# Kernel tuning notes

Measured on AMD Instinct MI355X. Metric: run time of the kernel, lower is better.

## Reference

```python
import jax, jax.numpy as jnp
import numpy as np

B, M, K = 32, 64, 36
DS, DX, DQ, H = 512, 128, 512, 256


def setup_inputs() -> dict:
    key = jax.random.key(0)
    ks = jax.random.split(key, 11)
    sc = lambda fan_in: 1.0 / np.sqrt(fan_in)
    return {
        "s2": jax.random.normal(ks[0], (B, M, DS), jnp.float32),
        "x0": jax.random.normal(ks[1], (B, K, DX), jnp.float32),
        "q": jax.random.normal(ks[2], (B, DQ), jnp.float32),
        # score MLP: Linear(DS+DX+DQ -> H), ReLU, Linear(H -> 1)
        "score_w1": jax.random.normal(ks[3], (DS + DX + DQ, H), jnp.float32) * sc(DS + DX + DQ),
        "score_b1": jax.random.normal(ks[4], (H,), jnp.float32) * 0.01,
        "score_w2": jax.random.normal(ks[5], (H, 1), jnp.float32) * sc(H),
        "score_b2": jax.random.normal(ks[6], (1,), jnp.float32) * 0.01,
        # h MLP: Linear(DS -> H), ReLU, Linear(H -> DX)
        "h_w1": jax.random.normal(ks[7], (DS, H), jnp.float32) * sc(DS),
        "h_b1": jax.random.normal(ks[8], (H,), jnp.float32) * 0.01,
        "h_w2": jax.random.normal(ks[9], (H, DX), jnp.float32) * sc(H),
        "h_b2": jax.random.normal(ks[10], (DX,), jnp.float32) * 0.01,
    }


def reference(s2, x0, q, score_w1, score_b1, score_w2, score_b2, h_w1, h_b1, h_w2, h_b2):
    ds = s2.shape[-1]
    dx = x0.shape[-1]
    # First score Linear over concat [s_exp, x_exp, q_exp] decomposes into
    # block matmuls (same math as Linear on the concat, no 4D concat tensor).
    w_s = score_w1[:ds]            # (DS, H)
    w_x = score_w1[ds:ds + dx]     # (DX, H)
    w_q = score_w1[ds + dx:]       # (DQ, H)
    pre_s = jnp.einsum('bmd,dh->bmh', s2, w_s)   # (b, m, H)
    pre_x = jnp.einsum('bkd,dh->bkh', x0, w_x)   # (b, k, H)
    pre_q = q @ w_q                              # (b, H)
    hidden = jax.nn.relu(pre_s[:, :, None, :] + pre_x[:, None, :, :]
                         + pre_q[:, None, None, :] + score_b1)  # (b, m, k, H)
    logits = jnp.einsum('bmkh,h->bmk', hidden, score_w2[:, 0]) + score_b2[0]
    att = jax.nn.softmax(logits, axis=1)         # softmax over m
    h_s = jax.nn.relu(s2 @ h_w1 + h_b1) @ h_w2 + h_b2  # (b, m, DX)
    agg = jnp.einsum('bmk,bmf->bkf', att, h_s)   # (b, k, DX)
    return jnp.concatenate([x0, agg], axis=-1)   # (b, k, 2*DX)
```

## Files before the change

### kernel.cpp

```cpp
#include <hip/hip_runtime.h>

#define B_  32
#define M_  64
#define K_  36
#define DS_ 512
#define DX_ 128
#define DQ_ 512
#define H_  256

#define S2B 1024
#define PXB 288
#define QPB 32

__global__ __launch_bounds__(512, 6) void kern1(
    const float* __restrict__ s2,
    const float* __restrict__ x0,
    const float* __restrict__ q,
    const float* __restrict__ score_w1,
    const float* __restrict__ score_b1,
    const float* __restrict__ h_w1,
    const float* __restrict__ h_b1,
    const float* __restrict__ h_w2,
    float* __restrict__ pre_s,
    float* __restrict__ px,
    float* __restrict__ qpre,
    float* __restrict__ hs)
{
    __shared__ float As[4 * DS_];
    __shared__ float comb[4 * H_];
    __shared__ float hre[4 * H_];

    const int t   = threadIdx.x;
    const int bid = blockIdx.x;
    const int h   = t & 255;
    const int kh  = __builtin_amdgcn_readfirstlane(t >> 8);

    if (bid < S2B) {
        const int tile = bid >> 1, mat = bid & 1;
        const float* W = mat ? h_w1 : score_w1;

        {
            const float* Asrc = s2 + (size_t)tile * 4 * DS_;
            *(float4*)&As[t * 4] = *(const float4*)(Asrc + t * 4);
        }
        __syncthreads();

        const float* Wp = W + (size_t)(kh * 256) * H_ + h;
        const int ab = kh * 256;

        float acc[4];
        #pragma unroll
        for (int r = 0; r < 4; ++r) acc[r] = 0.f;

        #pragma unroll 8
        for (int k = 0; k < 256; k += 4) {
            const float b0 = Wp[(size_t)(k + 0) * H_];
            const float b1 = Wp[(size_t)(k + 1) * H_];
            const float b2 = Wp[(size_t)(k + 2) * H_];
            const float b3 = Wp[(size_t)(k + 3) * H_];
            #pragma unroll
            for (int r = 0; r < 4; ++r) {
                const float4 a = *(const float4*)&As[r * DS_ + ab + k];
                acc[r] = fmaf(a.x, b0, acc[r]);
                acc[r] = fmaf(a.y, b1, acc[r]);
                acc[r] = fmaf(a.z, b2, acc[r]);
                acc[r] = fmaf(a.w, b3, acc[r]);
            }
        }

        if (kh) {
            #pragma unroll
            for (int r = 0; r < 4; ++r) comb[r * H_ + h] = acc[r];
        }
        __syncthreads();

        if (!mat) {
            if (!kh) {
                float* dst = pre_s + (size_t)tile * 4 * H_ + h;
                #pragma unroll
                for (int r = 0; r < 4; ++r)
                    dst[(size_t)r * H_] = acc[r] + comb[r * H_ + h];
            }
        } else {
            if (!kh) {
                const float b1v = h_b1[h];
                #pragma unroll
                for (int r = 0; r < 4; ++r)
                    hre[r * H_ + h] =
                        fmaxf(acc[r] + comb[r * H_ + h] + b1v, 0.f);
            }
            __syncthreads();

            const int row = t >> 7;
            const int f   = t & 127;
            const float* w2p = h_w2 + f;
            float o0 = 0.f, o1 = 0.f, o2 = 0.f, o3 = 0.f;
            #pragma unroll 4
            for (int k = 0; k < H_; k += 4) {
                o0 = fmaf(hre[row * H_ + k + 0], w2p[(size_t)(k + 0) * DX_], o0);
                o1 = fmaf(hre[row * H_ + k + 1], w2p[(size_t)(k + 1) * DX_], o1);
                o2 = fmaf(hre[row * H_ + k + 2], w2p[(size_t)(k + 2) * DX_], o2);
                o3 = fmaf(hre[row * H_ + k + 3], w2p[(size_t)(k + 3) * DX_], o3);
            }
            hs[((size_t)tile * 4 + row) * DX_ + f] = (o0 + o1) + (o2 + o3);
        }

    } else if (bid < S2B + PXB) {
        const int tile = bid - S2B;

        if (t < 128) {
            const float* Asrc = x0 + (size_t)tile * 4 * DX_;
            *(float4*)&As[t * 4] = *(const float4*)(Asrc + t * 4);
        }
        __syncthreads();

        const float* Wp = score_w1 + (size_t)(DS_ + kh * 64) * H_ + h;
        const int ab = kh * 64;

        float acc[4];
        #pragma unroll
        for (int r = 0; r < 4; ++r) acc[r] = 0.f;

        #pragma unroll 4
        for (int k = 0; k < 64; k += 4) {
            const float b0 = Wp[(size_t)(k + 0) * H_];
            const float b1 = Wp[(size_t)(k + 1) * H_];
            const float b2 = Wp[(size_t)(k + 2) * H_];
            const float b3 = Wp[(size_t)(k + 3) * H_];
            #pragma unroll
            for (int r = 0; r < 4; ++r) {
                const float4 a = *(const float4*)&As[r * DX_ + ab + k];
                acc[r] = fmaf(a.x, b0, acc[r]);
                acc[r] = fmaf(a.y, b1, acc[r]);
                acc[r] = fmaf(a.z, b2, acc[r]);
                acc[r] = fmaf(a.w, b3, acc[r]);
            }
        }
        if (kh) {
            #pragma unroll
            for (int r = 0; r < 4; ++r) comb[r * H_ + h] = acc[r];
        }
        __syncthreads();
        if (!kh) {
            const float b1v = score_b1[h];
            float* dst = px + (size_t)tile * 4 * H_ + h;
            #pragma unroll
            for (int r = 0; r < 4; ++r)
                dst[(size_t)r * H_] = acc[r] + comb[r * H_ + h] + b1v;
        }

    } else {
        const int b = bid - (S2B + PXB);

        if (t < 128) {
            const float* Asrc = q + (size_t)b * DQ_;
            *(float4*)&As[t * 4] = *(const float4*)(Asrc + t * 4);
        }
        __syncthreads();

        const float* wq = score_w1 + (size_t)(DS_ + DX_ + kh * 256) * H_ + h;
        const int qb = kh * 256;
        float a0 = 0.f, a1 = 0.f, a2 = 0.f, a3 = 0.f;
        #pragma unroll 8
        for (int d = 0; d < 256; d += 4) {
            const float4 q4 = *(const float4*)&As[qb + d];
            a0 = fmaf(q4.x, wq[(size_t)(d + 0) * H_], a0);
            a1 = fmaf(q4.y, wq[(size_t)(d + 1) * H_], a1);
            a2 = fmaf(q4.z, wq[(size_t)(d + 2) * H_], a2);
            a3 = fmaf(q4.w, wq[(size_t)(d + 3) * H_], a3);
        }
        const float s = (a0 + a1) + (a2 + a3);
        if (kh) comb[h] = s;
        __syncthreads();
        if (!kh) qpre[(size_t)b * H_ + h] = s + comb[h];
    }
}

__global__ __launch_bounds__(256) void kern3(
    const float* __restrict__ pre_s,
    const float* __restrict__ px,
    const float* __restrict__ qpre,
    const float* __restrict__ score_w2,
    const float* __restrict__ hs,
    const float* __restrict__ h_b2,
    const float* __restrict__ x0,
    float* __restrict__ out)
{
    __shared__ float logit[M_];
    __shared__ float att[M_];
    __shared__ float pr[DX_];

    const int t    = threadIdx.x;
    const int bk   = blockIdx.x;
    const int b    = bk / K_;
    const int lane = t & 63, wave = t >> 6;
    const int hq   = lane << 2;

    float4 c4, v4;
    {
        const float4 qv = *(const float4*)(qpre + (size_t)b * H_ + hq);
        const float4 pv = *(const float4*)(px + (size_t)bk * H_ + hq);
        c4.x = qv.x + pv.x; c4.y = qv.y + pv.y;
        c4.z = qv.z + pv.z; c4.w = qv.w + pv.w;
        v4 = *(const float4*)(score_w2 + hq);
    }

    const float* ps = pre_s + (size_t)b * M_ * H_;
    #pragma unroll 4
    for (int mi = 0; mi < 16; ++mi) {
        const int m = wave * 16 + mi;
        const float4 p = *(const float4*)(ps + (size_t)m * H_ + hq);
        float x = fmaxf(p.x + c4.x, 0.f) * v4.x
                + fmaxf(p.y + c4.y, 0.f) * v4.y
                + fmaxf(p.z + c4.z, 0.f) * v4.z
                + fmaxf(p.w + c4.w, 0.f) * v4.w;
        #pragma unroll
        for (int off = 32; off > 0; off >>= 1)
            x += __shfl_xor(x, off, 64);
        if (lane == 0) logit[m] = x;
    }
    __syncthreads();

    if (wave == 0) {
        const float L = logit[lane];
        float mx = L;
        #pragma unroll
        for (int off = 32; off > 0; off >>= 1)
            mx = fmaxf(mx, __shfl_xor(mx, off, 64));
        const float e = expf(L - mx);
        float sm = e;
        #pragma unroll
        for (int off = 32; off > 0; off >>= 1)
            sm += __shfl_xor(sm, off, 64);
        att[lane] = e / sm;
    }
    __syncthreads();

    const int f = t & 127, mh = t >> 7;
    {
        const float* hsp = hs + ((size_t)b * M_ + mh * 32) * DX_ + f;
        float r = 0.f;
        #pragma unroll 4
        for (int m2 = 0; m2 < 32; ++m2)
            r = fmaf(att[mh * 32 + m2], hsp[(size_t)m2 * DX_], r);
        if (mh) pr[f] = r;
        __syncthreads();
        if (!mh)
            out[(size_t)bk * (2 * DX_) + DX_ + f] = r + pr[f] + h_b2[f];
    }
    if (t < DX_)
        out[(size_t)bk * (2 * DX_) + t] = x0[(size_t)bk * DX_ + t];
}

extern "C" void kernel_launch(void* const* d_in, const int* in_sizes, int n_in,
                              void* d_out, int out_size, void* d_ws, size_t ws_size,
                              hipStream_t stream) {
    (void)in_sizes; (void)n_in; (void)out_size; (void)ws_size;
    const float* s2       = (const float*)d_in[0];
    const float* x0       = (const float*)d_in[1];
    const float* q        = (const float*)d_in[2];
    const float* score_w1 = (const float*)d_in[3];
    const float* score_b1 = (const float*)d_in[4];
    const float* score_w2 = (const float*)d_in[5];
    const float* h_w1     = (const float*)d_in[7];
    const float* h_b1     = (const float*)d_in[8];
    const float* h_w2     = (const float*)d_in[9];
    const float* h_b2     = (const float*)d_in[10];
    float* out = (float*)d_out;

    float* ws    = (float*)d_ws;
    float* pre_s = ws;
    float* px    = pre_s + (size_t)B_ * M_ * H_;
    float* qpre  = px    + (size_t)B_ * K_ * H_;
    float* hs    = qpre  + (size_t)B_ * H_;

    kern1<<<S2B + PXB + QPB, 512, 0, stream>>>(
        s2, x0, q, score_w1, score_b1, h_w1, h_b1, h_w2,
        pre_s, px, qpre, hs);
    kern3<<<B_ * K_, 256, 0, stream>>>(pre_s, px, qpre, score_w2, hs, h_b2,
                                       x0, out);
}
```

Measured before the change: 134.2 us.

## Retile s2 projection to 8 rows per block with 8-way split-K reduction

The s2 GEMM blocks now process 8 rows instead of 4, halving the block count. Each thread computes a 4-wide column strip using float4 weight loads, and the K dimension is split across 8 wavefronts with an LDS reduction. This doubles weight reuse per block and cuts global weight traffic. The costs are more registers (occupancy bound lowered to 4), a large 64KB+ LDS buffer, and an extra reduction pass. The h_w2 second layer is also restructured so each thread produces two outputs with float2 loads.

```diff
diff --git a/kernel.cpp b/kernel.cpp
--- a/kernel.cpp
+++ b/kernel.cpp
@@ -8,11 +8,11 @@
 #define DQ_ 512
 #define H_  256
 
-#define S2B 1024
+#define S2B 512
 #define PXB 288
 #define QPB 32
 
-__global__ __launch_bounds__(512, 6) void kern1(
+__global__ __launch_bounds__(512, 4) void kern1(
     const float* __restrict__ s2,
     const float* __restrict__ x0,
     const float* __restrict__ q,
@@ -26,91 +26,115 @@
     float* __restrict__ qpre,
     float* __restrict__ hs)
 {
-    __shared__ float As[4 * DS_];
-    __shared__ float comb[4 * H_];
-    __shared__ float hre[4 * H_];
+    __shared__ float lds[16384];
+    __shared__ float hre[8 * H_];
 
     const int t   = threadIdx.x;
     const int bid = blockIdx.x;
-    const int h   = t & 255;
-    const int kh  = __builtin_amdgcn_readfirstlane(t >> 8);
+    const int l   = t & 63;
+    const int w   = __builtin_amdgcn_readfirstlane(t >> 6);
 
     if (bid < S2B) {
         const int tile = bid >> 1, mat = bid & 1;
-        const float* W = mat ? h_w1 : score_w1;
+        const float* Wm = mat ? h_w1 : score_w1;
 
         {
-            const float* Asrc = s2 + (size_t)tile * 4 * DS_;
-            *(float4*)&As[t * 4] = *(const float4*)(Asrc + t * 4);
-        }
-        __syncthreads();
-
-        const float* Wp = W + (size_t)(kh * 256) * H_ + h;
-        const int ab = kh * 256;
-
-        float acc[4];
-        #pragma unroll
-        for (int r = 0; r < 4; ++r) acc[r] = 0.f;
-
-        #pragma unroll 8
-        for (int k = 0; k < 256; k += 4) {
-            const float b0 = Wp[(size_t)(k + 0) * H_];
-            const float b1 = Wp[(size_t)(k + 1) * H_];
-            const float b2 = Wp[(size_t)(k + 2) * H_];
-            const float b3 = Wp[(size_t)(k + 3) * H_];
+            const float* Asrc = s2 + (size_t)tile * 8 * DS_;
+            *(float4*)&lds[t * 4]        = *(const float4*)(Asrc + t * 4);
+            *(float4*)&lds[t * 4 + 2048] = *(const float4*)(Asrc + t * 4 + 2048);
+        }
+        __syncthreads();
+
+        const float4* Wq = (const float4*)Wm + l;
+        const int k0 = w * 64;
+
+        float4 acc[8];
+        #pragma unroll
+        for (int r = 0; r < 8; ++r) acc[r] = make_float4(0.f, 0.f, 0.f, 0.f);
+
+        #pragma unroll 2
+        for (int kq = 0; kq < 16; ++kq) {
+            const int k = k0 + kq * 4;
+            const float4 w0  = Wq[(size_t)(k + 0) * 64];
+            const float4 w1  = Wq[(size_t)(k + 1) * 64];
+            const float4 w2v = Wq[(size_t)(k + 2) * 64];
+            const float4 w3  = Wq[(size_t)(k + 3) * 64];
             #pragma unroll
-            for (int r = 0; r < 4; ++r) {
-                const float4 a = *(const float4*)&As[r * DS_ + ab + k];
-                acc[r] = fmaf(a.x, b0, acc[r]);
-                acc[r] = fmaf(a.y, b1, acc[r]);
-                acc[r] = fmaf(a.z, b2, acc[r]);
-                acc[r] = fmaf(a.w, b3, acc[r]);
+            for (int r = 0; r < 8; ++r) {
+                const float4 a = *(const float4*)&lds[r * DS_ + k];
+                acc[r].x = fmaf(a.x, w0.x, acc[r].x);
+                acc[r].y = fmaf(a.x, w0.y, acc[r].y);
+                acc[r].z = fmaf(a.x, w0.z, acc[r].z);
+                acc[r].w = fmaf(a.x, w0.w, acc[r].w);
+                acc[r].x = fmaf(a.y, w1.x, acc[r].x);
+                acc[r].y = fmaf(a.y, w1.y, acc[r].y);
+                acc[r].z = fmaf(a.y, w1.z, acc[r].z);
+                acc[r].w = fmaf(a.y, w1.w, acc[r].w);
+                acc[r].x = fmaf(a.z, w2v.x, acc[r].x);
+                acc[r].y = fmaf(a.z, w2v.y, acc[r].y);
+                acc[r].z = fmaf(a.z, w2v.z, acc[r].z);
+                acc[r].w = fmaf(a.z, w2v.w, acc[r].w);
+                acc[r].x = fmaf(a.w, w3.x, acc[r].x);
+                acc[r].y = fmaf(a.w, w3.y, acc[r].y);
+                acc[r].z = fmaf(a.w, w3.z, acc[r].z);
+                acc[r].w = fmaf(a.w, w3.w, acc[r].w);
             }
         }
-
-        if (kh) {
-            #pragma unroll
-            for (int r = 0; r < 4; ++r) comb[r * H_ + h] = acc[r];
-        }
-        __syncthreads();
+        __syncthreads();
+
+        #pragma unroll
+        for (int r = 0; r < 8; ++r)
+            *(float4*)&lds[w * 2048 + r * 256 + l * 4] = acc[r];
+        __syncthreads();
+
+        float4 s = *(const float4*)&lds[w * 256 + l * 4];
+        #pragma unroll
+        for (int ww = 1; ww < 8; ++ww) {
+            const float4 p = *(const float4*)&lds[ww * 2048 + w * 256 + l * 4];
+            s.x += p.x; s.y += p.y; s.z += p.z; s.w += p.w;
+        }
 
         if (!mat) {
-            if (!kh) {
-                float* dst = pre_s + (size_t)tile * 4 * H_ + h;
-                #pragma unroll
-                for (int r = 0; r < 4; ++r)
-                    dst[(size_t)r * H_] = acc[r] + comb[r * H_ + h];
+            *(float4*)(pre_s + ((size_t)tile * 8 + w) * H_ + l * 4) = s;
+        } else {
+            const float4 bv = *(const float4*)(h_b1 + l * 4);
+            float4 o;
+            o.x = fmaxf(s.x + bv.x, 0.f);
+            o.y = fmaxf(s.y + bv.y, 0.f);
+            o.z = fmaxf(s.z + bv.z, 0.f);
+            o.w = fmaxf(s.w + bv.w, 0.f);
+            *(float4*)&hre[w * H_ + l * 4] = o;
+            __syncthreads();
+
+            const int row = w;
+            const int f0  = l * 2;
+            const float* w2p = h_w2 + f0;
+            float s0 = 0.f, s1 = 0.f;
+            #pragma unroll 2
+            for (int k = 0; k < H_; k += 4) {
+                const float4 hv = *(const float4*)&hre[row * H_ + k];
+                const float2 wa = *(const float2*)(w2p + (size_t)(k + 0) * DX_);
+                const float2 wb = *(const float2*)(w2p + (size_t)(k + 1) * DX_);
+                const float2 wc = *(const float2*)(w2p + (size_t)(k + 2) * DX_);
+                const float2 wd = *(const float2*)(w2p + (size_t)(k + 3) * DX_);
+                s0 = fmaf(hv.x, wa.x, s0); s1 = fmaf(hv.x, wa.y, s1);
+                s0 = fmaf(hv.y, wb.x, s0); s1 = fmaf(hv.y, wb.y, s1);
+                s0 = fmaf(hv.z, wc.x, s0); s1 = fmaf(hv.z, wc.y, s1);
+                s0 = fmaf(hv.w, wd.x, s0); s1 = fmaf(hv.w, wd.y, s1);
             }
-        } else {
-            if (!kh) {
-                const float b1v = h_b1[h];
-                #pragma unroll
-                for (int r = 0; r < 4; ++r)
-                    hre[r * H_ + h] =
-                        fmaxf(acc[r] + comb[r * H_ + h] + b1v, 0.f);
-            }
-            __syncthreads();
-
-            const int row = t >> 7;
-            const int f   = t & 127;
-            const float* w2p = h_w2 + f;
-            float o0 = 0.f, o1 = 0.f, o2 = 0.f, o3 = 0.f;
-            #pragma unroll 4
-            for (int k = 0; k < H_; k += 4) {
-                o0 = fmaf(hre[row * H_ + k + 0], w2p[(size_t)(k + 0) * DX_], o0);
-                o1 = fmaf(hre[row * H_ + k + 1], w2p[(size_t)(k + 1) * DX_], o1);
-                o2 = fmaf(hre[row * H_ + k + 2], w2p[(size_t)(k + 2) * DX_], o2);
-                o3 = fmaf(hre[row * H_ + k + 3], w2p[(size_t)(k + 3) * DX_], o3);
-            }
-            hs[((size_t)tile * 4 + row) * DX_ + f] = (o0 + o1) + (o2 + o3);
+            *(float2*)(hs + ((size_t)tile * 8 + row) * DX_ + f0) =
+                make_float2(s0, s1);
         }
 
     } else if (bid < S2B + PXB) {
         const int tile = bid - S2B;
+        const int h    = t & 255;
+        const int kh   = __builtin_amdgcn_readfirstlane(t >> 8);
+        float* comb = &lds[4096];
 
         if (t < 128) {
             const float* Asrc = x0 + (size_t)tile * 4 * DX_;
-            *(float4*)&As[t * 4] = *(const float4*)(Asrc + t * 4);
+            *(float4*)&lds[t * 4] = *(const float4*)(Asrc + t * 4);
         }
         __syncthreads();
 
@@ -129,7 +153,7 @@
             const float b3 = Wp[(size_t)(k + 3) * H_];
             #pragma unroll
             for (int r = 0; r < 4; ++r) {
-                const float4 a = *(const float4*)&As[r * DX_ + ab + k];
+                const float4 a = *(const float4*)&lds[r * DX_ + ab + k];
                 acc[r] = fmaf(a.x, b0, acc[r]);
                 acc[r] = fmaf(a.y, b1, acc[r]);
                 acc[r] = fmaf(a.z, b2, acc[r]);
@@ -151,19 +175,22 @@
 
     } else {
         const int b = bid - (S2B + PXB);
+        const int h = t & 255;
+        const int kh = __builtin_amdgcn_readfirstlane(t >> 8);
+        float* comb = &lds[4096];
 
         if (t < 128) {
             const float* Asrc = q + (size_t)b * DQ_;
-            *(float4*)&As[t * 4] = *(const float4*)(Asrc + t * 4);
+            *(float4*)&lds[t * 4] = *(const float4*)(Asrc + t * 4);
         }
         __syncthreads();
 
         const float* wq = score_w1 + (size_t)(DS_ + DX_ + kh * 256) * H_ + h;
         const int qb = kh * 256;
         float a0 = 0.f, a1 = 0.f, a2 = 0.f, a3 = 0.f;
-        #pragma unroll 8
+        #pragma unroll 4
         for (int d = 0; d < 256; d += 4) {
-            const float4 q4 = *(const float4*)&As[qb + d];
+            const float4 q4 = *(const float4*)&lds[qb + d];
             a0 = fmaf(q4.x, wq[(size_t)(d + 0) * H_], a0);
             a1 = fmaf(q4.y, wq[(size_t)(d + 1) * H_], a1);
             a2 = fmaf(q4.z, wq[(size_t)(d + 2) * H_], a2);
```

After: 135.6 us. Within noise of the previous version (+1.0%).
